# Performance work log

Measured on AMD Instinct MI355X. Metric: run time of the kernel, lower is better.

## Reference

```python
import jax, jax.numpy as jnp
import numpy as np

IN, OUT, RANK = 4096, 4096, 16
ALPHA = 1.0


def setup_inputs() -> dict:
    key = jax.random.key(0)
    ks = jax.random.split(key, 5)
    x = jax.random.normal(ks[0], (4, 2048, IN), dtype=jnp.float32)
    W = jax.random.normal(ks[1], (OUT, IN), dtype=jnp.float32) * 0.02
    bias = jax.random.normal(ks[2], (OUT,), dtype=jnp.float32) * 0.02
    A = jax.random.normal(ks[3], (RANK, IN), dtype=jnp.float32) * (1.0 / RANK)
    B = jax.random.normal(ks[4], (OUT, RANK), dtype=jnp.float32) * 0.02
    return {"x": x, "W": W, "bias": bias, "A": A, "B": B}


def reference(x, W, bias, A, B):
    # base linear: out = x @ W.T + bias
    out = jnp.einsum('bsi,oi->bso', x, W) + bias
    # LoRA delta applied in low-rank form (same math as F.linear(x, B@A*scale))
    scale = ALPHA / RANK
    xa = jnp.einsum('bsi,ri->bsr', x, A)          # [B,S,rank]
    out = out + jnp.einsum('bsr,or->bso', xa, B) * scale
    return out
```

## Files before the change

### kernel.cpp

```cpp
#include <hip/hip_runtime.h>
#include <hip/hip_bf16.h>
#include <stdint.h>

#define MDIM 8192
#define NDIM 4096
#define KDIM 4096

#define BM 128
#define BN 128
#define BK 64

typedef short bf16x8 __attribute__((ext_vector_type(8)));
typedef float floatx4 __attribute__((ext_vector_type(4)));

__device__ __forceinline__ unsigned short f2bf(float f) {
    union { __hip_bfloat16 h; unsigned short u; } v;
    v.h = __float2bfloat16(f);
    return v.u;
}

__device__ __forceinline__ float bf2f(unsigned short u) {
    union { unsigned int i; float f; } v;
    v.i = ((unsigned int)u) << 16;
    return v.f;
}

__global__ __launch_bounds__(256) void cvt_bf16(
    const float* __restrict__ in, unsigned short* __restrict__ out, int n8) {
    int idx = blockIdx.x * blockDim.x + threadIdx.x;
    int stride = gridDim.x * blockDim.x;
    for (int i = idx; i < n8; i += stride) {
        const float4* p = (const float4*)in + (size_t)i * 2;
        float4 a = p[0], b = p[1];
        bf16x8 o;
        o[0] = (short)f2bf(a.x); o[1] = (short)f2bf(a.y);
        o[2] = (short)f2bf(a.z); o[3] = (short)f2bf(a.w);
        o[4] = (short)f2bf(b.x); o[5] = (short)f2bf(b.y);
        o[6] = (short)f2bf(b.z); o[7] = (short)f2bf(b.w);
        *((bf16x8*)out + i) = o;
    }
}

__global__ __launch_bounds__(256) void lora_xa(
    const unsigned short* __restrict__ xc,
    const float* __restrict__ A,
    const float* __restrict__ Bf,
    unsigned short* __restrict__ xa,
    unsigned short* __restrict__ Bc) {
    const int gt = blockIdx.x * blockDim.x + threadIdx.x;
    if (gt < 8192) {
        const float4* p = (const float4*)Bf + (size_t)gt * 2;
        float4 a = p[0], b = p[1];
        bf16x8 o;
        o[0] = (short)f2bf(a.x); o[1] = (short)f2bf(a.y);
        o[2] = (short)f2bf(a.z); o[3] = (short)f2bf(a.w);
        o[4] = (short)f2bf(b.x); o[5] = (short)f2bf(b.y);
        o[6] = (short)f2bf(b.z); o[7] = (short)f2bf(b.w);
        *((bf16x8*)Bc + gt) = o;
    }

    const int lane = threadIdx.x & 63;
    const int wave = gt >> 6;
    const int m0 = wave * 4;
    if (m0 >= MDIM) return;

    float acc[4][16];
#pragma unroll
    for (int q = 0; q < 4; ++q)
#pragma unroll
        for (int r = 0; r < 16; ++r) acc[q][r] = 0.f;

    for (int k = lane * 4; k < KDIM; k += 256) {
        float xf[4][4];
#pragma unroll
        for (int q = 0; q < 4; ++q) {
            short4 xv = *(const short4*)(xc + (size_t)(m0 + q) * KDIM + k);
            xf[q][0] = bf2f((unsigned short)xv.x);
            xf[q][1] = bf2f((unsigned short)xv.y);
            xf[q][2] = bf2f((unsigned short)xv.z);
            xf[q][3] = bf2f((unsigned short)xv.w);
        }
#pragma unroll
        for (int r = 0; r < 16; ++r) {
            float4 av = *(const float4*)(A + (size_t)r * KDIM + k);
#pragma unroll
            for (int q = 0; q < 4; ++q)
                acc[q][r] += xf[q][0] * av.x + xf[q][1] * av.y +
                             xf[q][2] * av.z + xf[q][3] * av.w;
        }
    }
#pragma unroll
    for (int q = 0; q < 4; ++q)
#pragma unroll
        for (int r = 0; r < 16; ++r) {
#pragma unroll
            for (int off = 32; off > 0; off >>= 1)
                acc[q][r] += __shfl_xor(acc[q][r], off, 64);
        }
    if (lane == 0) {
        const float scale = 1.0f / 16.0f;
#pragma unroll
        for (int q = 0; q < 4; ++q)
#pragma unroll
            for (int r = 0; r < 16; ++r)
                xa[(size_t)(m0 + q) * 16 + r] = f2bf(acc[q][r] * scale);
    }
}

__global__ __launch_bounds__(256, 4) void lora_gemm(
    const unsigned short* __restrict__ x,
    const unsigned short* __restrict__ W,
    const float* __restrict__ bias,
    const unsigned short* __restrict__ Bl,
    const unsigned short* __restrict__ xa,
    float* __restrict__ out) {
    __shared__ __align__(16) unsigned short lA[BM * BK];
    __shared__ __align__(16) unsigned short lB[BN * BK];

    const int bn = blockIdx.x * BN;
    const int bm = blockIdx.y * BM;
    const int t = threadIdx.x;
    const int lane = t & 63;
    const int wave = t >> 6;
    const int wm = (wave >> 1) * 64;
    const int wn = (wave & 1) * 64;
    const int fr = lane & 15;
    const int fq = lane >> 4;
    const int f7 = fr & 7;

    const int srow = lane >> 3;
    const int scc = (lane & 7) ^ srow;

    floatx4 acc[4][4];
#pragma unroll
    for (int i = 0; i < 4; ++i)
#pragma unroll
        for (int j = 0; j < 4; ++j)
            acc[i][j] = (floatx4){0.f, 0.f, 0.f, 0.f};

    {
        bf16x8 z = {0, 0, 0, 0, 0, 0, 0, 0};
        bf16x8 af[4], bfv[4];
#pragma unroll
        for (int i = 0; i < 4; ++i) {
            int row = bm + wm + i * 16 + fr;
            af[i] = (fq < 2) ? *(const bf16x8*)(xa + (size_t)row * 16 + fq * 8) : z;
        }
#pragma unroll
        for (int j = 0; j < 4; ++j) {
            int row = bn + wn + j * 16 + fr;
            bfv[j] = (fq < 2) ? *(const bf16x8*)(Bl + (size_t)row * 16 + fq * 8) : z;
        }
#pragma unroll
        for (int i = 0; i < 4; ++i)
#pragma unroll
            for (int j = 0; j < 4; ++j)
                acc[i][j] = __builtin_amdgcn_mfma_f32_16x16x32_bf16(af[i], bfv[j], acc[i][j], 0, 0, 0);
    }

    for (int k0 = 0; k0 < KDIM; k0 += BK) {
#pragma unroll
        for (int i = 0; i < 4; ++i) {
            int cbase = i * 256 + wave * 64;
            int row = (cbase >> 3) + srow;
            __builtin_amdgcn_global_load_lds(
                (const __attribute__((address_space(1))) unsigned int*)(x + (size_t)(bm + row) * KDIM + k0 + scc * 8),
                (__attribute__((address_space(3))) unsigned int*)&lA[cbase * 8], 16, 0, 0);
            __builtin_amdgcn_global_load_lds(
                (const __attribute__((address_space(1))) unsigned int*)(W + (size_t)(bn + row) * KDIM + k0 + scc * 8),
                (__attribute__((address_space(3))) unsigned int*)&lB[cbase * 8], 16, 0, 0);
        }
        __syncthreads();

#pragma unroll
        for (int kk = 0; kk < BK; kk += 32) {
            const int jb = kk >> 3;
            bf16x8 af[4], bfv[4];
#pragma unroll
            for (int i = 0; i < 4; ++i) {
                int r = wm + i * 16 + fr;
                af[i] = *(const bf16x8*)&lA[r * BK + (((jb + fq) ^ f7) << 3)];
            }
#pragma unroll
            for (int j = 0; j < 4; ++j) {
                int r = wn + j * 16 + fr;
                bfv[j] = *(const bf16x8*)&lB[r * BK + (((jb + fq) ^ f7) << 3)];
            }
#pragma unroll
            for (int i = 0; i < 4; ++i)
#pragma unroll
                for (int j = 0; j < 4; ++j)
                    acc[i][j] = __builtin_amdgcn_mfma_f32_16x16x32_bf16(af[i], bfv[j], acc[i][j], 0, 0, 0);
        }
        __syncthreads();
    }

#pragma unroll
    for (int j = 0; j < 4; ++j) {
        int col = bn + wn + j * 16 + fr;
        float bv = bias[col];
#pragma unroll
        for (int i = 0; i < 4; ++i) {
            int row0 = bm + wm + i * 16 + fq * 4;
#pragma unroll
            for (int r = 0; r < 4; ++r) {
                out[(size_t)(row0 + r) * NDIM + col] = acc[i][j][r] + bv;
            }
        }
    }
}

extern "C" void kernel_launch(void* const* d_in, const int* in_sizes, int n_in,
                              void* d_out, int out_size, void* d_ws, size_t ws_size,
                              hipStream_t stream) {
    const float* x    = (const float*)d_in[0];
    const float* W    = (const float*)d_in[1];
    const float* bias = (const float*)d_in[2];
    const float* A    = (const float*)d_in[3];
    const float* Bf   = (const float*)d_in[4];
    float* out = (float*)d_out;

    unsigned short* xc = (unsigned short*)d_ws;
    unsigned short* Wc = xc + (size_t)MDIM * KDIM;
    unsigned short* xa = Wc + (size_t)NDIM * KDIM;
    unsigned short* Bc = xa + (size_t)MDIM * 16;

    cvt_bf16<<<8192, 256, 0, stream>>>(x, xc, (MDIM * KDIM) / 8);
    cvt_bf16<<<4096, 256, 0, stream>>>(W, Wc, (NDIM * KDIM) / 8);
    lora_xa<<<512, 256, 0, stream>>>(xc, A, Bf, xa, Bc);
    lora_gemm<<<dim3(NDIM / BN, MDIM / BM), 256, 0, stream>>>(xc, Wc, bias, Bc, xa, out);
}
```

Before: 554.8 us.

## Enlarge GEMM tiles to 256x256 with double-buffered LDS pipeline and swizzled grid

The main GEMM moves from 128x128 tiles with 4 waves to 256x256 tiles with 8 waves. The K loop is split into four sub-phases that interleave async global-to-LDS staging of the next tile with MFMA compute. Double-buffered LDS, explicit waitcnt and barriers, setprio, and a workgroup-index remap for L2 locality are intended to hide memory latency and raise arithmetic intensity. The larger tile needs 128 KB of LDS and more accumulators, which cuts occupancy and raises register pressure.

```diff
diff --git a/kernel.cpp b/kernel.cpp
--- a/kernel.cpp
+++ b/kernel.cpp
@@ -6,8 +6,8 @@
 #define NDIM 4096
 #define KDIM 4096
 
-#define BM 128
-#define BN 128
+#define BM 256
+#define BN 256
 #define BK 64
 
 typedef short bf16x8 __attribute__((ext_vector_type(8)));
@@ -107,42 +107,62 @@
     }
 }
 
-__global__ __launch_bounds__(256, 4) void lora_gemm(
+__device__ __forceinline__ void stage_half(
+    const unsigned short* __restrict__ gp, unsigned short* lb,
+    int row0, int kt, int h, int wave, int srow, int scc) {
+#pragma unroll
+    for (int l = 0; l < 2; ++l) {
+        const int cbase = h * 1024 + l * 512 + wave * 64;
+        const int row = (cbase >> 3) + srow;
+        __builtin_amdgcn_global_load_lds(
+            (const __attribute__((address_space(1))) unsigned int*)(gp + (size_t)(row0 + row) * KDIM + kt * BK + scc * 8),
+            (__attribute__((address_space(3))) unsigned int*)&lb[cbase * 8], 16, 0, 0);
+    }
+}
+
+__global__ __launch_bounds__(512, 2) void lora_gemm(
     const unsigned short* __restrict__ x,
     const unsigned short* __restrict__ W,
     const float* __restrict__ bias,
     const unsigned short* __restrict__ Bl,
     const unsigned short* __restrict__ xa,
     float* __restrict__ out) {
-    __shared__ __align__(16) unsigned short lA[BM * BK];
-    __shared__ __align__(16) unsigned short lB[BN * BK];
-
-    const int bn = blockIdx.x * BN;
-    const int bm = blockIdx.y * BM;
+    __shared__ __align__(16) unsigned short lA[2][BM * BK];
+    __shared__ __align__(16) unsigned short lB[2][BN * BK];
+
+    int wg = blockIdx.y * 16 + blockIdx.x;
+    wg = (wg & 7) * 64 + (wg >> 3);
+    const int bn = (wg & 15) * BN;
+    const int bm = (wg >> 4) * BM;
+
     const int t = threadIdx.x;
     const int lane = t & 63;
     const int wave = t >> 6;
-    const int wm = (wave >> 1) * 64;
-    const int wn = (wave & 1) * 64;
+    const int wm = (wave >> 2) * 128;
+    const int wn = (wave & 3) * 64;
     const int fr = lane & 15;
     const int fq = lane >> 4;
     const int f7 = fr & 7;
-
     const int srow = lane >> 3;
     const int scc = (lane & 7) ^ srow;
 
-    floatx4 acc[4][4];
-#pragma unroll
-    for (int i = 0; i < 4; ++i)
+    const int sl0 = (fq ^ f7) << 3;
+    const int sl1 = ((4 + fq) ^ f7) << 3;
+    const int aoff = (wm + fr) * BK;
+    const int boff = (wn + fr) * BK;
+
+    floatx4 acc[8][4];
+#pragma unroll
+    for (int i = 0; i < 8; ++i)
 #pragma unroll
         for (int j = 0; j < 4; ++j)
             acc[i][j] = (floatx4){0.f, 0.f, 0.f, 0.f};
 
     {
         bf16x8 z = {0, 0, 0, 0, 0, 0, 0, 0};
-        bf16x8 af[4], bfv[4];
-#pragma unroll
-        for (int i = 0; i < 4; ++i) {
+        bf16x8 af[8], bfv[4];
+#pragma unroll
+        for (int i = 0; i < 8; ++i) {
             int row = bm + wm + i * 16 + fr;
             af[i] = (fq < 2) ? *(const bf16x8*)(xa + (size_t)row * 16 + fq * 8) : z;
         }
@@ -152,47 +172,99 @@
             bfv[j] = (fq < 2) ? *(const bf16x8*)(Bl + (size_t)row * 16 + fq * 8) : z;
         }
 #pragma unroll
-        for (int i = 0; i < 4; ++i)
+        for (int i = 0; i < 8; ++i)
 #pragma unroll
             for (int j = 0; j < 4; ++j)
                 acc[i][j] = __builtin_amdgcn_mfma_f32_16x16x32_bf16(af[i], bfv[j], acc[i][j], 0, 0, 0);
     }
 
-    for (int k0 = 0; k0 < KDIM; k0 += BK) {
-#pragma unroll
-        for (int i = 0; i < 4; ++i) {
-            int cbase = i * 256 + wave * 64;
-            int row = (cbase >> 3) + srow;
-            __builtin_amdgcn_global_load_lds(
-                (const __attribute__((address_space(1))) unsigned int*)(x + (size_t)(bm + row) * KDIM + k0 + scc * 8),
-                (__attribute__((address_space(3))) unsigned int*)&lA[cbase * 8], 16, 0, 0);
-            __builtin_amdgcn_global_load_lds(
-                (const __attribute__((address_space(1))) unsigned int*)(W + (size_t)(bn + row) * KDIM + k0 + scc * 8),
-                (__attribute__((address_space(3))) unsigned int*)&lB[cbase * 8], 16, 0, 0);
-        }
-        __syncthreads();
-
-#pragma unroll
-        for (int kk = 0; kk < BK; kk += 32) {
-            const int jb = kk >> 3;
-            bf16x8 af[4], bfv[4];
-#pragma unroll
-            for (int i = 0; i < 4; ++i) {
-                int r = wm + i * 16 + fr;
-                af[i] = *(const bf16x8*)&lA[r * BK + (((jb + fq) ^ f7) << 3)];
-            }
-#pragma unroll
-            for (int j = 0; j < 4; ++j) {
-                int r = wn + j * 16 + fr;
-                bfv[j] = *(const bf16x8*)&lB[r * BK + (((jb + fq) ^ f7) << 3)];
-            }
-#pragma unroll
-            for (int i = 0; i < 4; ++i)
-#pragma unroll
-                for (int j = 0; j < 4; ++j)
-                    acc[i][j] = __builtin_amdgcn_mfma_f32_16x16x32_bf16(af[i], bfv[j], acc[i][j], 0, 0, 0);
-        }
-        __syncthreads();
+    stage_half(x, lA[0], bm, 0, 0, wave, srow, scc);
+    stage_half(x, lA[0], bm, 0, 1, wave, srow, scc);
+    stage_half(W, lB[0], bn, 0, 0, wave, srow, scc);
+    stage_half(W, lB[0], bn, 0, 1, wave, srow, scc);
+    stage_half(W, lB[1], bn, 1, 0, wave, srow, scc);
+    stage_half(W, lB[1], bn, 1, 1, wave, srow, scc);
+    asm volatile("s_waitcnt vmcnt(4)" ::: "memory");
+    __builtin_amdgcn_s_barrier();
+
+#pragma unroll 2
+    for (int n = 0; n < KDIM / BK; ++n) {
+        const int cur = n & 1;
+        const unsigned short* la = lA[cur];
+        const unsigned short* lb = lB[cur];
+        bf16x8 bF0[4], bF1[4], aA[4], aB[4], aC[4], aD[4];
+
+#pragma unroll
+        for (int j = 0; j < 4; ++j)
+            bF0[j] = *(const bf16x8*)&lb[boff + j * 16 * BK + sl0];
+#pragma unroll
+        for (int i = 0; i < 4; ++i)
+            aA[i] = *(const bf16x8*)&la[aoff + i * 16 * BK + sl0];
+        if (n < 63) stage_half(x, lA[cur ^ 1], bm, n + 1, 0, wave, srow, scc);
+        __builtin_amdgcn_s_barrier();
+        asm volatile("s_waitcnt lgkmcnt(0)" ::: "memory");
+        __builtin_amdgcn_sched_barrier(0);
+        __builtin_amdgcn_s_setprio(1);
+#pragma unroll
+        for (int i = 0; i < 4; ++i)
+#pragma unroll
+            for (int j = 0; j < 4; ++j)
+                acc[i][j] = __builtin_amdgcn_mfma_f32_16x16x32_bf16(aA[i], bF0[j], acc[i][j], 0, 0, 0);
+        __builtin_amdgcn_s_setprio(0);
+        __builtin_amdgcn_s_barrier();
+
+#pragma unroll
+        for (int j = 0; j < 4; ++j)
+            bF1[j] = *(const bf16x8*)&lb[boff + j * 16 * BK + sl1];
+#pragma unroll
+        for (int i = 0; i < 4; ++i)
+            aB[i] = *(const bf16x8*)&la[aoff + i * 16 * BK + sl1];
+        if (n < 63) stage_half(x, lA[cur ^ 1], bm, n + 1, 1, wave, srow, scc);
+        __builtin_amdgcn_s_barrier();
+        asm volatile("s_waitcnt lgkmcnt(0)" ::: "memory");
+        __builtin_amdgcn_sched_barrier(0);
+        __builtin_amdgcn_s_setprio(1);
+#pragma unroll
+        for (int i = 0; i < 4; ++i)
+#pragma unroll
+            for (int j = 0; j < 4; ++j)
+                acc[i][j] = __builtin_amdgcn_mfma_f32_16x16x32_bf16(aB[i], bF1[j], acc[i][j], 0, 0, 0);
+        __builtin_amdgcn_s_setprio(0);
+        __builtin_amdgcn_s_barrier();
+
+#pragma unroll
+        for (int i = 0; i < 4; ++i)
+            aC[i] = *(const bf16x8*)&la[aoff + 64 * BK + i * 16 * BK + sl0];
+        if (n < 62) stage_half(W, lB[cur], bn, n + 2, 0, wave, srow, scc);
+        __builtin_amdgcn_s_barrier();
+        asm volatile("s_waitcnt lgkmcnt(0)" ::: "memory");
+        __builtin_amdgcn_sched_barrier(0);
+        __builtin_amdgcn_s_setprio(1);
+#pragma unroll
+        for (int i = 0; i < 4; ++i)
+#pragma unroll
+            for (int j = 0; j < 4; ++j)
+                acc[4 + i][j] = __builtin_amdgcn_mfma_f32_16x16x32_bf16(aC[i], bF0[j], acc[4 + i][j], 0, 0, 0);
+        __builtin_amdgcn_s_setprio(0);
+        __builtin_amdgcn_s_barrier();
+
+#pragma unroll
+        for (int i = 0; i < 4; ++i)
+            aD[i] = *(const bf16x8*)&la[aoff + 64 * BK + i * 16 * BK + sl1];
+        if (n < 62) stage_half(W, lB[cur], bn, n + 2, 1, wave, srow, scc);
+        if (n < 62) { asm volatile("s_waitcnt vmcnt(4)" ::: "memory"); }
+        else        { asm volatile("s_waitcnt vmcnt(0)" ::: "memory"); }
+        __builtin_amdgcn_s_barrier();
+        asm volatile("s_waitcnt lgkmcnt(0)" ::: "memory");
+        __builtin_amdgcn_sched_barrier(0);
+        __builtin_amdgcn_s_setprio(1);
+#pragma unroll
+        for (int i = 0; i < 4; ++i)
+#pragma unroll
+            for (int j = 0; j < 4; ++j)
+                acc[4 + i][j] = __builtin_amdgcn_mfma_f32_16x16x32_bf16(aD[i], bF1[j], acc[4 + i][j], 0, 0, 0);
+        __builtin_amdgcn_s_setprio(0);
+        __builtin_amdgcn_s_barrier();
     }
 
 #pragma unroll
@@ -200,7 +272,7 @@
         int col = bn + wn + j * 16 + fr;
         float bv = bias[col];
 #pragma unroll
-        for (int i = 0; i < 4; ++i) {
+        for (int i = 0; i < 8; ++i) {
             int row0 = bm + wm + i * 16 + fq * 4;
 #pragma unroll
             for (int r = 0; r < 4; ++r) {
@@ -228,5 +300,5 @@
     cvt_bf16<<<8192, 256, 0, stream>>>(x, xc, (MDIM * KDIM) / 8);
     cvt_bf16<<<4096, 256, 0, stream>>>(W, Wc, (NDIM * KDIM) / 8);
     lora_xa<<<512, 256, 0, stream>>>(xc, A, Bf, xa, Bc);
-    lora_gemm<<<dim3(NDIM / BN, MDIM / BM), 256, 0, stream>>>(xc, Wc, bias, Bc, xa, out);
-}
+    lora_gemm<<<dim3(NDIM / BN, MDIM / BM), 512, 0, stream>>>(xc, Wc, bias, Bc, xa, out);
+}
```

Measured after the change: 552.0 us. No clear change (-0.5%).

## Fuse bf16 conversions and LoRA xa into one pre-kernel; remap GEMM tiles

Applied to the files above, without the earlier changes.

Replaces the three preprocessing launches (x convert, W convert, xa plus B convert) with one kernel. Its first blocks compute xa directly from fp32 x and the rest convert x, W and B to bf16 with a grid-stride loop. Because xa no longer waits on the bf16 copy of x, it can run alongside the conversion, and two launches plus one kernel boundary go away. The xa blocks now read fp32 x, twice the bytes of the bf16 copy. The GEMM block index is also remapped so that blocks which are close in dispatch order are spread across row tiles, which may change L2 or XCD locality.

```diff
diff --git a/kernel.cpp b/kernel.cpp
--- a/kernel.cpp
+++ b/kernel.cpp
@@ -9,6 +9,9 @@
 #define BM 128
 #define BN 128
 #define BK 64
+
+#define XA_BLOCKS 512
+#define CVT_BLOCKS 6144
 
 typedef short bf16x8 __attribute__((ext_vector_type(8)));
 typedef float floatx4 __attribute__((ext_vector_type(4)));
@@ -19,91 +22,82 @@
     return v.u;
 }
 
-__device__ __forceinline__ float bf2f(unsigned short u) {
-    union { unsigned int i; float f; } v;
-    v.i = ((unsigned int)u) << 16;
-    return v.f;
-}
-
-__global__ __launch_bounds__(256) void cvt_bf16(
-    const float* __restrict__ in, unsigned short* __restrict__ out, int n8) {
-    int idx = blockIdx.x * blockDim.x + threadIdx.x;
-    int stride = gridDim.x * blockDim.x;
-    for (int i = idx; i < n8; i += stride) {
-        const float4* p = (const float4*)in + (size_t)i * 2;
-        float4 a = p[0], b = p[1];
+__global__ __launch_bounds__(256) void fused_pre(
+    const float* __restrict__ x,
+    const float* __restrict__ Wf,
+    const float* __restrict__ Bf,
+    const float* __restrict__ A,
+    unsigned short* __restrict__ xc,
+    unsigned short* __restrict__ Wc,
+    unsigned short* __restrict__ Bc,
+    unsigned short* __restrict__ xa) {
+    const int b = blockIdx.x;
+
+    if (b < XA_BLOCKS) {
+        const int lane = threadIdx.x & 63;
+        const int wave = (b * 256 + (int)threadIdx.x) >> 6;
+        const int m0 = wave * 4;
+
+        float acc[4][16];
+#pragma unroll
+        for (int q = 0; q < 4; ++q)
+#pragma unroll
+            for (int r = 0; r < 16; ++r) acc[q][r] = 0.f;
+
+        for (int k = lane * 4; k < KDIM; k += 256) {
+            float4 xv[4];
+#pragma unroll
+            for (int q = 0; q < 4; ++q)
+                xv[q] = *(const float4*)(x + (size_t)(m0 + q) * KDIM + k);
+#pragma unroll
+            for (int r = 0; r < 16; ++r) {
+                float4 av = *(const float4*)(A + (size_t)r * KDIM + k);
+#pragma unroll
+                for (int q = 0; q < 4; ++q)
+                    acc[q][r] += xv[q].x * av.x + xv[q].y * av.y +
+                                 xv[q].z * av.z + xv[q].w * av.w;
+            }
+        }
+#pragma unroll
+        for (int q = 0; q < 4; ++q)
+#pragma unroll
+            for (int r = 0; r < 16; ++r) {
+#pragma unroll
+                for (int off = 32; off > 0; off >>= 1)
+                    acc[q][r] += __shfl_xor(acc[q][r], off, 64);
+            }
+        if (lane == 0) {
+            const float scale = 1.0f / 16.0f;
+#pragma unroll
+            for (int q = 0; q < 4; ++q)
+#pragma unroll
+                for (int r = 0; r < 16; ++r)
+                    xa[(size_t)(m0 + q) * 16 + r] = f2bf(acc[q][r] * scale);
+        }
+        return;
+    }
+
+    const int NX = (MDIM * KDIM) / 8;
+    const int NW = (NDIM * KDIM) / 8;
+    const int NB = (NDIM * 16) / 8;
+    const int total = NX + NW + NB;
+    int idx = (b - XA_BLOCKS) * 256 + (int)threadIdx.x;
+    const int stride = CVT_BLOCKS * 256;
+    for (int i = idx; i < total; i += stride) {
+        const float* src;
+        unsigned short* dst;
+        int off;
+        if (i < NX)           { src = x;  dst = xc; off = i; }
+        else if (i < NX + NW) { src = Wf; dst = Wc; off = i - NX; }
+        else                  { src = Bf; dst = Bc; off = i - NX - NW; }
+        const float4* p = (const float4*)src + (size_t)off * 2;
+        float4 a = p[0], c = p[1];
         bf16x8 o;
         o[0] = (short)f2bf(a.x); o[1] = (short)f2bf(a.y);
         o[2] = (short)f2bf(a.z); o[3] = (short)f2bf(a.w);
-        o[4] = (short)f2bf(b.x); o[5] = (short)f2bf(b.y);
-        o[6] = (short)f2bf(b.z); o[7] = (short)f2bf(b.w);
-        *((bf16x8*)out + i) = o;
-    }
-}
-
-__global__ __launch_bounds__(256) void lora_xa(
-    const unsigned short* __restrict__ xc,
-    const float* __restrict__ A,
-    const float* __restrict__ Bf,
-    unsigned short* __restrict__ xa,
-    unsigned short* __restrict__ Bc) {
-    const int gt = blockIdx.x * blockDim.x + threadIdx.x;
-    if (gt < 8192) {
-        const float4* p = (const float4*)Bf + (size_t)gt * 2;
-        float4 a = p[0], b = p[1];
-        bf16x8 o;
-        o[0] = (short)f2bf(a.x); o[1] = (short)f2bf(a.y);
-        o[2] = (short)f2bf(a.z); o[3] = (short)f2bf(a.w);
-        o[4] = (short)f2bf(b.x); o[5] = (short)f2bf(b.y);
-        o[6] = (short)f2bf(b.z); o[7] = (short)f2bf(b.w);
-        *((bf16x8*)Bc + gt) = o;
-    }
-
-    const int lane = threadIdx.x & 63;
-    const int wave = gt >> 6;
-    const int m0 = wave * 4;
-    if (m0 >= MDIM) return;
-
-    float acc[4][16];
-#pragma unroll
-    for (int q = 0; q < 4; ++q)
-#pragma unroll
-        for (int r = 0; r < 16; ++r) acc[q][r] = 0.f;
-
-    for (int k = lane * 4; k < KDIM; k += 256) {
-        float xf[4][4];
-#pragma unroll
-        for (int q = 0; q < 4; ++q) {
-            short4 xv = *(const short4*)(xc + (size_t)(m0 + q) * KDIM + k);
-            xf[q][0] = bf2f((unsigned short)xv.x);
-            xf[q][1] = bf2f((unsigned short)xv.y);
-            xf[q][2] = bf2f((unsigned short)xv.z);
-            xf[q][3] = bf2f((unsigned short)xv.w);
-        }
-#pragma unroll
-        for (int r = 0; r < 16; ++r) {
-            float4 av = *(const float4*)(A + (size_t)r * KDIM + k);
-#pragma unroll
-            for (int q = 0; q < 4; ++q)
-                acc[q][r] += xf[q][0] * av.x + xf[q][1] * av.y +
-                             xf[q][2] * av.z + xf[q][3] * av.w;
-        }
-    }
-#pragma unroll
-    for (int q = 0; q < 4; ++q)
-#pragma unroll
-        for (int r = 0; r < 16; ++r) {
-#pragma unroll
-            for (int off = 32; off > 0; off >>= 1)
-                acc[q][r] += __shfl_xor(acc[q][r], off, 64);
-        }
-    if (lane == 0) {
-        const float scale = 1.0f / 16.0f;
-#pragma unroll
-        for (int q = 0; q < 4; ++q)
-#pragma unroll
-            for (int r = 0; r < 16; ++r)
-                xa[(size_t)(m0 + q) * 16 + r] = f2bf(acc[q][r] * scale);
+        o[4] = (short)f2bf(c.x); o[5] = (short)f2bf(c.y);
+        o[6] = (short)f2bf(c.z); o[7] = (short)f2bf(c.w);
+        *((bf16x8*)dst + off) = o;
     }
 }
 
@@ -117,8 +111,11 @@
     __shared__ __align__(16) unsigned short lA[BM * BK];
     __shared__ __align__(16) unsigned short lB[BN * BK];
 
-    const int bn = blockIdx.x * BN;
-    const int bm = blockIdx.y * BM;
+    int id = blockIdx.y * 32 + blockIdx.x;
+    id = (id & 7) * 256 + (id >> 3);
+    const int bn = (id & 31) * BN;
+    const int bm = (id >> 5) * BM;
+
     const int t = threadIdx.x;
     const int lane = t & 63;
     const int wave = t >> 6;
@@ -225,8 +222,6 @@
     unsigned short* xa = Wc + (size_t)NDIM * KDIM;
     unsigned short* Bc = xa + (size_t)MDIM * 16;
 
-    cvt_bf16<<<8192, 256, 0, stream>>>(x, xc, (MDIM * KDIM) / 8);
-    cvt_bf16<<<4096, 256, 0, stream>>>(W, Wc, (NDIM * KDIM) / 8);
-    lora_xa<<<512, 256, 0, stream>>>(xc, A, Bf, xa, Bc);
+    fused_pre<<<XA_BLOCKS + CVT_BLOCKS, 256, 0, stream>>>(x, W, Bf, A, xc, Wc, Bc, xa);
     lora_gemm<<<dim3(NDIM / BN, MDIM / BM), 256, 0, stream>>>(xc, Wc, bias, Bc, xa, out);
 }
```

New measurement: 596.9 us. 1.08x slower.
